# Kernel optimization log

Measured on AMD Instinct MI355X. Metric: run time of the kernel, lower is better.

Reference implementation:

```python
import jax, jax.numpy as jnp
import numpy as np

D = 4096
B = 2
S = 2048


def setup_inputs() -> dict:
    key = jax.random.key(0)
    k1, k2, k3, k4 = jax.random.split(key, 4)
    x = jax.random.normal(k1, (B, S, D), dtype=jnp.float32)
    # 2-bit symmetric quantized codes stored as uint8 in torch; torch's
    # clamp(-1,1).to(uint8) wraps -1 -> 255, so codes span {0,1,255}-like
    # values. We draw the full uint8 range for a representative baseline.
    q_int = jax.random.randint(k2, (D, D), 0, 256, dtype=jnp.int32)
    # per-channel positive scales (small, like 2-bit scales: |w|max / 1)
    scale = jax.random.uniform(k3, (D,), dtype=jnp.float32) * 0.01 + 1e-4
    # symmetric quantization -> zero_point = 0 per channel (int buffer)
    zero_point = jnp.zeros((D,), dtype=jnp.int32)
    bias = jax.random.normal(k4, (D,), dtype=jnp.float32) * 0.02
    return {"x": x, "q_int": q_int, "scale": scale,
            "zero_point": zero_point, "bias": bias}


def reference(x, q_int, scale, zero_point, bias):
    # Faithful to FFQLinear.forward:
    #   weight = (q_int.float() - zero_point) * scale
    # NOTE: no unsqueeze(-1) here (unlike pack time), so scale/zp broadcast
    # over the LAST (column) axis of the [d, d] code matrix.
    zp = zero_point.astype(jnp.float32)
    W = (q_int.astype(jnp.float32) - zp[None, :]) * scale[None, :]  # [D, D]
    b, s, d = x.shape
    # F.linear(x2d, W.t(), bias) == x2d @ W + bias
    out = jnp.einsum('bsd,dk->bsk', x, W) + bias  # [B, S, D]
    return out
```

## Files before the change

kernel.cpp:

```cpp
#include <hip/hip_runtime.h>
#include <stdint.h>

typedef unsigned short u16;
typedef __attribute__((ext_vector_type(8))) short short8;
typedef __attribute__((ext_vector_type(4))) float f32x4;

#define D_DIM 4096
#define M_DIM 4096
#define K_DIM 4096
#define N_DIM 4096

#define BM 128
#define BN 128
#define BK 64

typedef const __attribute__((address_space(1))) void* gas1_t;
typedef __attribute__((address_space(3))) void* las3_t;

__device__ __forceinline__ void g2l16(const void* g, void* l) {
  __builtin_amdgcn_global_load_lds((gas1_t)g, (las3_t)l, 16, 0, 0);
}

__device__ __forceinline__ u16 f2bf(float f) {
  uint32_t u = __float_as_uint(f);
  uint32_t r = (u + 0x7FFFu + ((u >> 16) & 1u)) >> 16;
  return (u16)r;
}

__global__ void cvt_x(const float* __restrict__ x, u16* __restrict__ xb) {
  int64_t base = ((int64_t)blockIdx.x * blockDim.x + threadIdx.x) * 16;
  float4 f[4];
#pragma unroll
  for (int j = 0; j < 4; ++j) f[j] = *(const float4*)(x + base + j * 4);
  union { u16 u[16]; uint4 q[2]; } o;
#pragma unroll
  for (int j = 0; j < 4; ++j) {
    o.u[4 * j + 0] = f2bf(f[j].x);
    o.u[4 * j + 1] = f2bf(f[j].y);
    o.u[4 * j + 2] = f2bf(f[j].z);
    o.u[4 * j + 3] = f2bf(f[j].w);
  }
  *(uint4*)(xb + base) = o.q[0];
  *(uint4*)(xb + base + 8) = o.q[1];
}

__global__ void cvt_q(const int* __restrict__ q, const int* __restrict__ zp,
                      u16* __restrict__ qt) {
  __shared__ u16 L[64][68];
  const int n0 = blockIdx.x * 64;
  const int k0 = blockIdx.y * 64;
  const int lc = threadIdx.x & 15;
  const int lr = threadIdx.x >> 4;

  const int z0 = zp[n0 + lc * 4 + 0];
  const int z1 = zp[n0 + lc * 4 + 1];
  const int z2 = zp[n0 + lc * 4 + 2];
  const int z3 = zp[n0 + lc * 4 + 3];

#pragma unroll
  for (int p = 0; p < 4; ++p) {
    int row = lr + p * 16;
    int4 v = *(const int4*)(q + (int64_t)(k0 + row) * D_DIM + n0 + lc * 4);
    L[row][lc * 4 + 0] = f2bf((float)(v.x - z0));
    L[row][lc * 4 + 1] = f2bf((float)(v.y - z1));
    L[row][lc * 4 + 2] = f2bf((float)(v.z - z2));
    L[row][lc * 4 + 3] = f2bf((float)(v.w - z3));
  }
  __syncthreads();

  const int kq = threadIdx.x & 7;
  const int nn = threadIdx.x >> 3;
#pragma unroll
  for (int p = 0; p < 2; ++p) {
    int n = nn + p * 32;
    union { u16 u[8]; uint4 v; } o;
#pragma unroll
    for (int i = 0; i < 8; ++i) o.u[i] = L[kq * 8 + i][n];
    *(uint4*)(qt + (int64_t)(n0 + n) * K_DIM + k0 + kq * 8) = o.v;
  }
}

__global__ __launch_bounds__(256, 3)
void gemm_kernel(const u16* __restrict__ A, const u16* __restrict__ Bt,
                 const float* __restrict__ scale, const float* __restrict__ bias,
                 float* __restrict__ C) {
  __shared__ u16 As[BM * BK];
  __shared__ u16 Bs[BN * BK];

  const int tid = threadIdx.x;
  const int bm0 = blockIdx.y * BM;
  const int bn0 = blockIdx.x * BN;

  const int lane = tid & 63;
  const int w = tid >> 6;
  const int wr = w >> 1, wc = w & 1;

  const int sRow = tid >> 3;
  const int sCol = (tid & 7) * 8;

  const u16* aG = A + (int64_t)(bm0 + sRow) * K_DIM + sCol;
  const u16* bG = Bt + (int64_t)(bn0 + sRow) * K_DIM + sCol;
  u16* aL = &As[tid * 8];
  u16* bL = &Bs[tid * 8];

  f32x4 acc[4][4];
#pragma unroll
  for (int m = 0; m < 4; ++m)
#pragma unroll
    for (int n = 0; n < 4; ++n) acc[m][n] = (f32x4)(0.f);

  const int l15 = lane & 15;
  const int lk = (lane >> 4) * 8;

  for (int kt = 0; kt < K_DIM; kt += BK) {
#pragma unroll
    for (int i = 0; i < 4; ++i)
      g2l16(aG + kt + (int64_t)i * 32 * K_DIM, aL + i * 2048);
#pragma unroll
    for (int i = 0; i < 4; ++i)
      g2l16(bG + kt + (int64_t)i * 32 * K_DIM, bL + i * 2048);
    __syncthreads();

#pragma unroll
    for (int kk = 0; kk < 2; ++kk) {
      short8 af[4], bf[4];
#pragma unroll
      for (int m = 0; m < 4; ++m)
        af[m] = *(const short8*)&As[(wr * 64 + m * 16 + l15) * BK + kk * 32 + lk];
#pragma unroll
      for (int n = 0; n < 4; ++n)
        bf[n] = *(const short8*)&Bs[(wc * 64 + n * 16 + l15) * BK + kk * 32 + lk];
#pragma unroll
      for (int m = 0; m < 4; ++m)
#pragma unroll
        for (int n = 0; n < 4; ++n)
          acc[m][n] = __builtin_amdgcn_mfma_f32_16x16x32_bf16(af[m], bf[n], acc[m][n], 0, 0, 0);
    }
    __syncthreads();
  }

  const int r0 = (lane >> 4) * 4;
#pragma unroll
  for (int n = 0; n < 4; ++n) {
    int col = bn0 + wc * 64 + n * 16 + l15;
    float sc = scale[col];
    float bs = bias[col];
#pragma unroll
    for (int m = 0; m < 4; ++m) {
      int row = bm0 + wr * 64 + m * 16 + r0;
#pragma unroll
      for (int j = 0; j < 4; ++j)
        C[(int64_t)(row + j) * N_DIM + col] = acc[m][n][j] * sc + bs;
    }
  }
}

extern "C" void kernel_launch(void* const* d_in, const int* in_sizes, int n_in,
                              void* d_out, int out_size, void* d_ws, size_t ws_size,
                              hipStream_t stream) {
  const float* x = (const float*)d_in[0];
  const int* q = (const int*)d_in[1];
  const float* scale = (const float*)d_in[2];
  const int* zp = (const int*)d_in[3];
  const float* bias = (const float*)d_in[4];
  float* out = (float*)d_out;

  u16* Xb = (u16*)d_ws;
  u16* Qt = Xb + (size_t)M_DIM * K_DIM;

  cvt_x<<<(M_DIM * (int64_t)K_DIM) / (256 * 16), 256, 0, stream>>>(x, Xb);

  dim3 gq(N_DIM / 64, K_DIM / 64);
  cvt_q<<<gq, 256, 0, stream>>>(q, zp, Qt);

  dim3 gg(N_DIM / BN, M_DIM / BM);
  gemm_kernel<<<gg, 256, 0, stream>>>(Xb, Qt, scale, bias, out);
}
```

Baseline: 327.3 us.

## Rewrite GEMM with 256x256 tiles, double-buffered LDS, swizzle and XCD remap

```diff
diff --git a/kernel.cpp b/kernel.cpp
--- a/kernel.cpp
+++ b/kernel.cpp
@@ -5,14 +5,7 @@
 typedef __attribute__((ext_vector_type(8))) short short8;
 typedef __attribute__((ext_vector_type(4))) float f32x4;
 
-#define D_DIM 4096
-#define M_DIM 4096
-#define K_DIM 4096
-#define N_DIM 4096
-
-#define BM 128
-#define BN 128
-#define BK 64
+#define KD 4096
 
 typedef const __attribute__((address_space(1))) void* gas1_t;
 typedef __attribute__((address_space(3))) void* las3_t;
@@ -23,48 +16,38 @@
 
 __device__ __forceinline__ u16 f2bf(float f) {
   uint32_t u = __float_as_uint(f);
-  uint32_t r = (u + 0x7FFFu + ((u >> 16) & 1u)) >> 16;
-  return (u16)r;
-}
-
-__global__ void cvt_x(const float* __restrict__ x, u16* __restrict__ xb) {
-  int64_t base = ((int64_t)blockIdx.x * blockDim.x + threadIdx.x) * 16;
-  float4 f[4];
-#pragma unroll
-  for (int j = 0; j < 4; ++j) f[j] = *(const float4*)(x + base + j * 4);
-  union { u16 u[16]; uint4 q[2]; } o;
-#pragma unroll
-  for (int j = 0; j < 4; ++j) {
-    o.u[4 * j + 0] = f2bf(f[j].x);
-    o.u[4 * j + 1] = f2bf(f[j].y);
-    o.u[4 * j + 2] = f2bf(f[j].z);
-    o.u[4 * j + 3] = f2bf(f[j].w);
-  }
-  *(uint4*)(xb + base) = o.q[0];
-  *(uint4*)(xb + base + 8) = o.q[1];
+  return (u16)((u + 0x7FFFu + ((u >> 16) & 1u)) >> 16);
+}
+
+__global__ void cvt_x(const float4* __restrict__ x, uint2* __restrict__ xb) {
+  int gid = blockIdx.x * 256 + threadIdx.x;
+  float4 f = x[gid];
+  union { u16 u[4]; uint2 v; } o;
+  o.u[0] = f2bf(f.x); o.u[1] = f2bf(f.y);
+  o.u[2] = f2bf(f.z); o.u[3] = f2bf(f.w);
+  xb[gid] = o.v;
 }
 
 __global__ void cvt_q(const int* __restrict__ q, const int* __restrict__ zp,
                       u16* __restrict__ qt) {
-  __shared__ u16 L[64][68];
+  __shared__ u16 Lt[64][66];
   const int n0 = blockIdx.x * 64;
   const int k0 = blockIdx.y * 64;
-  const int lc = threadIdx.x & 15;
-  const int lr = threadIdx.x >> 4;
-
-  const int z0 = zp[n0 + lc * 4 + 0];
-  const int z1 = zp[n0 + lc * 4 + 1];
-  const int z2 = zp[n0 + lc * 4 + 2];
-  const int z3 = zp[n0 + lc * 4 + 3];
+  const int nc = threadIdx.x & 15;
+  const int kr = threadIdx.x >> 4;
+
+  int z[4];
+#pragma unroll
+  for (int c = 0; c < 4; ++c) z[c] = zp[n0 + nc * 4 + c];
 
 #pragma unroll
   for (int p = 0; p < 4; ++p) {
-    int row = lr + p * 16;
-    int4 v = *(const int4*)(q + (int64_t)(k0 + row) * D_DIM + n0 + lc * 4);
-    L[row][lc * 4 + 0] = f2bf((float)(v.x - z0));
-    L[row][lc * 4 + 1] = f2bf((float)(v.y - z1));
-    L[row][lc * 4 + 2] = f2bf((float)(v.z - z2));
-    L[row][lc * 4 + 3] = f2bf((float)(v.w - z3));
+    int k = p * 16 + kr;
+    int4 v = *(const int4*)(q + (int64_t)(k0 + k) * KD + n0 + nc * 4);
+    Lt[k][nc * 4 + 0] = f2bf((float)(v.x - z[0]));
+    Lt[k][nc * 4 + 1] = f2bf((float)(v.y - z[1]));
+    Lt[k][nc * 4 + 2] = f2bf((float)(v.z - z[2]));
+    Lt[k][nc * 4 + 3] = f2bf((float)(v.w - z[3]));
   }
   __syncthreads();
 
@@ -75,82 +58,155 @@
     int n = nn + p * 32;
     union { u16 u[8]; uint4 v; } o;
 #pragma unroll
-    for (int i = 0; i < 8; ++i) o.u[i] = L[kq * 8 + i][n];
-    *(uint4*)(qt + (int64_t)(n0 + n) * K_DIM + k0 + kq * 8) = o.v;
-  }
-}
-
-__global__ __launch_bounds__(256, 3)
-void gemm_kernel(const u16* __restrict__ A, const u16* __restrict__ Bt,
-                 const float* __restrict__ scale, const float* __restrict__ bias,
-                 float* __restrict__ C) {
-  __shared__ u16 As[BM * BK];
-  __shared__ u16 Bs[BN * BK];
+    for (int i = 0; i < 8; ++i) o.u[i] = Lt[kq * 8 + i][n];
+    *(uint4*)(qt + (int64_t)(n0 + n) * KD + k0 + kq * 8) = o.v;
+  }
+}
+
+__global__ __launch_bounds__(512, 2)
+void gemm8(const u16* __restrict__ A, const u16* __restrict__ Bt,
+           const float* __restrict__ scale, const float* __restrict__ bias,
+           float* __restrict__ C) {
+  __shared__ u16 lds[65536];
 
   const int tid = threadIdx.x;
-  const int bm0 = blockIdx.y * BM;
-  const int bn0 = blockIdx.x * BN;
+  const int orig = blockIdx.x;
+  const int lid = (orig & 7) * 32 + (orig >> 3);
+  const int bm0 = (lid >> 4) * 256;
+  const int bn0 = (lid & 15) * 256;
 
   const int lane = tid & 63;
   const int w = tid >> 6;
-  const int wr = w >> 1, wc = w & 1;
-
-  const int sRow = tid >> 3;
-  const int sCol = (tid & 7) * 8;
-
-  const u16* aG = A + (int64_t)(bm0 + sRow) * K_DIM + sCol;
-  const u16* bG = Bt + (int64_t)(bn0 + sRow) * K_DIM + sCol;
-  u16* aL = &As[tid * 8];
-  u16* bL = &Bs[tid * 8];
-
-  f32x4 acc[4][4];
-#pragma unroll
-  for (int m = 0; m < 4; ++m)
+  const int wr = w >> 2;
+  const int wc = w & 3;
+  const int l15 = lane & 15;
+  const int q4 = lane >> 4;
+  const int l7 = l15 & 7;
+
+  const int rl = tid >> 3;
+  const int csw = (tid & 7) ^ (rl & 7);
+  const u16* gA = A + (int64_t)(bm0 + rl) * KD + csw * 8;
+  const u16* gB = Bt + (int64_t)(bn0 + rl) * KD + csw * 8;
+
+#define STA(b, qq, kt) g2l16(gA + (int64_t)(qq) * 64 * KD + (kt), &lds[(b) * 32768 + (qq) * 4096 + tid * 8])
+#define STB(b, qq, kt) g2l16(gB + (int64_t)(qq) * 64 * KD + (kt), &lds[16384 + (b) * 32768 + (qq) * 4096 + tid * 8])
+
+#define RD_A(mh)                                                              \
+  do {                                                                        \
+    _Pragma("unroll") for (int m = 0; m < 4; ++m) {                           \
+      const int row = wr * 128 + (mh) * 64 + m * 16 + l15;                    \
+      _Pragma("unroll") for (int kk = 0; kk < 2; ++kk)                        \
+        ar[m][kk] = *(const short8*)&Ab[row * 64 + (((kk * 4 + q4) ^ l7) * 8)]; \
+    }                                                                         \
+  } while (0)
+
+#define RD_B(nn0)                                                             \
+  do {                                                                        \
+    _Pragma("unroll") for (int n = 0; n < 2; ++n) {                           \
+      const int col = wc * 64 + ((nn0) + n) * 16 + l15;                       \
+      _Pragma("unroll") for (int kk = 0; kk < 2; ++kk)                        \
+        br[(nn0) + n][kk] = *(const short8*)&Bb[col * 64 + (((kk * 4 + q4) ^ l7) * 8)]; \
+    }                                                                         \
+  } while (0)
+
+#define MFMA_Q(mb, nn0)                                                       \
+  do {                                                                        \
+    __builtin_amdgcn_s_setprio(1);                                            \
+    _Pragma("unroll") for (int m = 0; m < 4; ++m)                             \
+      _Pragma("unroll") for (int n = 0; n < 2; ++n)                           \
+        _Pragma("unroll") for (int kk = 0; kk < 2; ++kk)                      \
+          acc[(mb) + m][(nn0) + n] = __builtin_amdgcn_mfma_f32_16x16x32_bf16( \
+              ar[m][kk], br[(nn0) + n][kk], acc[(mb) + m][(nn0) + n], 0, 0, 0); \
+    __builtin_amdgcn_s_setprio(0);                                            \
+  } while (0)
+
+#define LGKM0 asm volatile("s_waitcnt lgkmcnt(0)" ::: "memory")
+#define BAR __builtin_amdgcn_s_barrier()
+
+  f32x4 acc[8][4];
+#pragma unroll
+  for (int m = 0; m < 8; ++m)
 #pragma unroll
     for (int n = 0; n < 4; ++n) acc[m][n] = (f32x4)(0.f);
 
-  const int l15 = lane & 15;
-  const int lk = (lane >> 4) * 8;
-
-  for (int kt = 0; kt < K_DIM; kt += BK) {
-#pragma unroll
-    for (int i = 0; i < 4; ++i)
-      g2l16(aG + kt + (int64_t)i * 32 * K_DIM, aL + i * 2048);
-#pragma unroll
-    for (int i = 0; i < 4; ++i)
-      g2l16(bG + kt + (int64_t)i * 32 * K_DIM, bL + i * 2048);
-    __syncthreads();
-
-#pragma unroll
-    for (int kk = 0; kk < 2; ++kk) {
-      short8 af[4], bf[4];
-#pragma unroll
-      for (int m = 0; m < 4; ++m)
-        af[m] = *(const short8*)&As[(wr * 64 + m * 16 + l15) * BK + kk * 32 + lk];
-#pragma unroll
-      for (int n = 0; n < 4; ++n)
-        bf[n] = *(const short8*)&Bs[(wc * 64 + n * 16 + l15) * BK + kk * 32 + lk];
-#pragma unroll
-      for (int m = 0; m < 4; ++m)
-#pragma unroll
-        for (int n = 0; n < 4; ++n)
-          acc[m][n] = __builtin_amdgcn_mfma_f32_16x16x32_bf16(af[m], bf[n], acc[m][n], 0, 0, 0);
-    }
-    __syncthreads();
-  }
-
-  const int r0 = (lane >> 4) * 4;
+  short8 ar[4][2], br[4][2];
+
+  STB(0, 0, 0); STB(0, 1, 0); STB(0, 2, 0); STB(0, 3, 0);
+  STA(0, 0, 0); STA(0, 2, 0); STA(0, 1, 0); STA(0, 3, 0);
+  asm volatile("s_waitcnt vmcnt(2)" ::: "memory");
+  BAR;
+
+  int cur = 0;
+  for (int t = 0; t < 63; ++t) {
+    const int ktn = (t + 1) * 64;
+    const u16* __restrict__ Ab = &lds[cur * 32768];
+    const u16* __restrict__ Bb = &lds[16384 + cur * 32768];
+    const int nb = cur ^ 1;
+
+    RD_A(0);
+    RD_B(0);
+    STB(nb, 0, ktn); STB(nb, 1, ktn);
+    BAR; LGKM0;
+    MFMA_Q(0, 0);
+    BAR;
+
+    RD_B(2);
+    STB(nb, 2, ktn); STB(nb, 3, ktn);
+    asm volatile("s_waitcnt vmcnt(4)" ::: "memory");
+    BAR; LGKM0;
+    MFMA_Q(0, 2);
+    BAR;
+
+    RD_A(1);
+    STA(nb, 0, ktn); STA(nb, 2, ktn);
+    BAR; LGKM0;
+    MFMA_Q(4, 0);
+    BAR;
+
+    STA(nb, 1, ktn); STA(nb, 3, ktn);
+    asm volatile("s_waitcnt vmcnt(2)" ::: "memory");
+    BAR; LGKM0;
+    MFMA_Q(4, 2);
+    BAR;
+
+    cur ^= 1;
+  }
+
+  {
+    const u16* __restrict__ Ab = &lds[cur * 32768];
+    const u16* __restrict__ Bb = &lds[16384 + cur * 32768];
+    RD_A(0);
+    RD_B(0);
+    BAR; LGKM0;
+    MFMA_Q(0, 0);
+    BAR;
+
+    RD_B(2);
+    asm volatile("s_waitcnt vmcnt(0)" ::: "memory");
+    BAR; LGKM0;
+    MFMA_Q(0, 2);
+    BAR;
+
+    RD_A(1);
+    BAR; LGKM0;
+    MFMA_Q(4, 0);
+    BAR;
+
+    MFMA_Q(4, 2);
+  }
+
+  const int r4 = q4 * 4;
 #pragma unroll
   for (int n = 0; n < 4; ++n) {
-    int col = bn0 + wc * 64 + n * 16 + l15;
-    float sc = scale[col];
-    float bs = bias[col];
-#pragma unroll
-    for (int m = 0; m < 4; ++m) {
-      int row = bm0 + wr * 64 + m * 16 + r0;
+    const int col = bn0 + wc * 64 + n * 16 + l15;
+    const float sc = scale[col];
+    const float bs = bias[col];
+#pragma unroll
+    for (int mi = 0; mi < 8; ++mi) {
+      const int row = bm0 + wr * 128 + mi * 16 + r4;
 #pragma unroll
       for (int j = 0; j < 4; ++j)
-        C[(int64_t)(row + j) * N_DIM + col] = acc[m][n][j] * sc + bs;
+        C[(int64_t)(row + j) * KD + col] = acc[mi][n][j] * sc + bs;
     }
   }
 }
@@ -166,13 +222,12 @@
   float* out = (float*)d_out;
 
   u16* Xb = (u16*)d_ws;
-  u16* Qt = Xb + (size_t)M_DIM * K_DIM;
-
-  cvt_x<<<(M_DIM * (int64_t)K_DIM) / (256 * 16), 256, 0, stream>>>(x, Xb);
-
-  dim3 gq(N_DIM / 64, K_DIM / 64);
+  u16* Qt = Xb + (size_t)4096 * 4096;
+
+  cvt_x<<<16384, 256, 0, stream>>>((const float4*)x, (uint2*)Xb);
+
+  dim3 gq(4096 / 64, 4096 / 64);
   cvt_q<<<gq, 256, 0, stream>>>(q, zp, Qt);
 
-  dim3 gg(N_DIM / BN, M_DIM / BM);
-  gemm_kernel<<<gg, 256, 0, stream>>>(Xb, Qt, scale, bias, out);
-}
+  gemm8<<<256, 512, 0, stream>>>(Xb, Qt, scale, bias, out);
+}
```

Result: faster. 294.9 us (-9.9%).
